# Performance work log

Hardware: AMD Instinct MI355X
Metric: run time of the kernel (lower is better)

The kernel has to match this reference:

```python
import jax, jax.numpy as jnp
import numpy as np

# Llama-2-7B-like GQA attention, prefill over packed equal-length sequences
H = 4096      # hidden_size
NH = 32       # num_attention_heads
NKV = 8       # num_key_value_heads
HD = H // NH  # head_dim = 128
B = 4         # number of packed sequences
S = 1024      # seq_len per sequence
T = B * S     # total packed tokens
BASE = 10000.0  # rope_theta


def setup_inputs() -> dict:
    key = jax.random.key(0)
    ks = jax.random.split(key, 5)
    x = jax.random.normal(ks[0], (T, H), jnp.float32)
    positions = jnp.tile(jnp.arange(S, dtype=jnp.int32), B)  # per-seq positions
    kv_cache = jnp.zeros((1,), jnp.float32)  # placeholder (prefill: kv from current tokens)
    init = 0.02
    wq = jax.random.normal(ks[1], (NH * HD, H), jnp.float32) * init
    wk = jax.random.normal(ks[2], (NKV * HD, H), jnp.float32) * init
    wv = jax.random.normal(ks[3], (NKV * HD, H), jnp.float32) * init
    wo = jax.random.normal(ks[4], (H, NH * HD), jnp.float32) * init
    return {"x": x, "positions": positions, "kv_cache": kv_cache,
            "wq": wq, "wk": wk, "wv": wv, "wo": wo, "seq_len": S}


def _rope(xh, cos_b, sin_b):
    # xh: [T, Hh, D]; cos_b/sin_b: [T, 1, D] (freqs repeat-interleaved by 2)
    half = xh.shape[-1] // 2
    x_rot = jnp.concatenate([-xh[..., half:], xh[..., :half]], axis=-1)
    return xh * cos_b + x_rot * sin_b


def reference(x, positions, kv_cache, wq, wk, wv, wo, seq_len):
    Tn = x.shape[0]
    q = (x @ wq.T).reshape(Tn, NH, HD)
    k = (x @ wk.T).reshape(Tn, NKV, HD)
    v = (x @ wv.T).reshape(Tn, NKV, HD)
    # GQA: repeat_interleave kv heads
    rep = NH // NKV
    k = jnp.repeat(k, rep, axis=1)
    v = jnp.repeat(v, rep, axis=1)
    # RoPE tables (faithful to _precompute_freqs/_rotary_embeddings)
    inv_freq = 1.0 / (BASE ** (jnp.arange(0, HD, 2, dtype=jnp.float32) / HD))
    t = jnp.arange(seq_len, dtype=jnp.float32)
    freqs = t[:, None] * inv_freq[None, :]            # [S, D/2]
    cos, sin = jnp.cos(freqs), jnp.sin(freqs)
    pos = jnp.clip(positions.astype(jnp.int32), 0, seq_len - 1)
    cos_b = jnp.repeat(cos[pos], 2, axis=-1)[:, None, :]  # [T,1,D]
    sin_b = jnp.repeat(sin[pos], 2, axis=-1)[:, None, :]
    q = _rope(q, cos_b, sin_b)
    k = _rope(k, cos_b, sin_b)
    # Paged attention (prefill): causal attention within each packed sequence
    Bn = Tn // seq_len
    qb = q.reshape(Bn, seq_len, NH, HD)
    kb = k.reshape(Bn, seq_len, NH, HD)
    vb = v.reshape(Bn, seq_len, NH, HD)
    scores = jnp.einsum('bqhd,bkhd->bhqk', qb, kb) * (HD ** -0.5)
    causal = jnp.tril(jnp.ones((seq_len, seq_len), bool))
    scores = jnp.where(causal[None, None], scores, -jnp.inf)
    probs = jax.nn.softmax(scores, axis=-1)
    out = jnp.einsum('bhqk,bkhd->bqhd', probs, vb).reshape(Tn, NH * HD)
    return out @ wo.T
```

## Files before the change

### kernel.cpp

```cpp
#include <hip/hip_runtime.h>
#include <hip/hip_bf16.h>
#include <math.h>

#define T_TOK 4096
#define HID   4096
#define NHQ   32
#define NKVH  8
#define HDIM  128
#define SEQ   1024
#define NBATCH 4

typedef __attribute__((ext_vector_type(8))) short bf16x8;
typedef __attribute__((ext_vector_type(4))) float f32x4;
typedef __attribute__((ext_vector_type(16))) float f32x16;

__device__ __forceinline__ unsigned short f2bf(float f) {
  union { float f; unsigned int u; } x; x.f = f;
  unsigned int r = x.u + 0x7FFFu + ((x.u >> 16) & 1u);
  return (unsigned short)(r >> 16);
}

#define GLOAD_LDS16(gp, lp)                                                        \
  __builtin_amdgcn_global_load_lds(                                                \
      (__attribute__((address_space(1))) void*)(unsigned long long)(const void*)(gp), \
      (__attribute__((address_space(3))) void*)(unsigned long long)(const void*)(lp), \
      16, 0, 0)

__global__ __launch_bounds__(256) void cast_all_k(const float* __restrict__ x,
                                                  const float* __restrict__ wq,
                                                  const float* __restrict__ wk,
                                                  const float* __restrict__ wv,
                                                  const float* __restrict__ wo,
                                                  unsigned short* __restrict__ xb,
                                                  unsigned short* __restrict__ wqkv,
                                                  unsigned short* __restrict__ wob) {
  int i = blockIdx.x * 256 + threadIdx.x;
  const float* src; unsigned short* dst; int off;
  if (i < 4194304)       { src = x;  dst = xb;   off = i; }
  else if (i < 8388608)  { src = wq; dst = wqkv; off = i - 4194304; }
  else if (i < 9437184)  { src = wk; dst = wqkv + 16777216; off = i - 8388608; }
  else if (i < 10485760) { src = wv; dst = wqkv + 20971520; off = i - 9437184; }
  else                   { src = wo; dst = wob;  off = i - 10485760; }
  float4 f = ((const float4*)src)[off];
  ushort4 o;
  o.x = f2bf(f.x); o.y = f2bf(f.y); o.z = f2bf(f.z); o.w = f2bf(f.w);
  ((ushort4*)dst)[off] = o;
}

template<bool FUSED>
__global__ __launch_bounds__(256) void gemm_core(const unsigned short* __restrict__ A,
                                                 const unsigned short* __restrict__ B,
                                                 float* __restrict__ C,
                                                 const int* __restrict__ pos,
                                                 unsigned short* __restrict__ qr,
                                                 unsigned short* __restrict__ kr,
                                                 unsigned short* __restrict__ vbuf,
                                                 int N, int K) {
  __shared__ unsigned short As[128][64];
  __shared__ unsigned short Bs[128][64];
  const int tid  = threadIdx.x;
  const int lane = tid & 63;
  const int wave = tid >> 6;
  const int half = lane >> 5;
  const int r31  = lane & 31;
  const int wm   = (wave >> 1) * 64;
  const int cb   = (wave & 1) * 32;
  const long rowBase = (long)blockIdx.y * 128;
  const long colBase = (long)blockIdx.x * 128;

  f32x16 acc[2][2] = {};

  for (int k0 = 0; k0 < K; k0 += 64) {
    __syncthreads();
#pragma unroll
    for (int it = 0; it < 4; ++it) {
      int c = it * 256 + tid;
      int row = c >> 3;
      int sg = (c & 7) ^ (row & 7);
      int ldsoff = (it * 256 + wave * 64) * 8;
      GLOAD_LDS16(A + (rowBase + row) * K + k0 + sg * 8, ((unsigned short*)As) + ldsoff);
      GLOAD_LDS16(B + (colBase + row) * K + k0 + sg * 8, ((unsigned short*)Bs) + ldsoff);
    }
    __syncthreads();
#pragma unroll
    for (int kk = 0; kk < 4; ++kk) {
      bf16x8 af[2], bfr[2];
#pragma unroll
      for (int i = 0; i < 2; ++i) {
        int row = wm + i * 32 + r31;
        af[i] = *(const bf16x8*)(&As[row][((kk * 2 + half) ^ (row & 7)) * 8]);
      }
#pragma unroll
      for (int j = 0; j < 2; ++j) {
        int row = cb + j * 64 + r31;
        bfr[j] = *(const bf16x8*)(&Bs[row][((kk * 2 + half) ^ (row & 7)) * 8]);
      }
#pragma unroll
      for (int i = 0; i < 2; ++i)
#pragma unroll
        for (int j = 0; j < 2; ++j)
          acc[i][j] = __builtin_amdgcn_mfma_f32_32x32x16_bf16(af[i], bfr[j], acc[i][j], 0, 0, 0);
    }
  }

  if (!FUSED) {
#pragma unroll
    for (int i = 0; i < 2; ++i)
#pragma unroll
      for (int j = 0; j < 2; ++j) {
        long c = colBase + cb + j * 64 + r31;
#pragma unroll
        for (int reg = 0; reg < 16; ++reg) {
          long row = rowBase + wm + i * 32 + 4 * half + (reg & 3) + 8 * (reg >> 2);
          C[row * N + c] = acc[i][j][reg];
        }
      }
    return;
  }

  const int n0 = (int)colBase;
  unsigned short* dst;
  int rstride, colofs;
  bool dorope;
  if (n0 < 4096)       { dst = qr;   rstride = NHQ * HDIM;  colofs = n0;        dorope = true; }
  else if (n0 < 5120)  { dst = kr;   rstride = NKVH * HDIM; colofs = n0 - 4096; dorope = true; }
  else                 { dst = vbuf; rstride = NKVH * HDIM; colofs = n0 - 5120; dorope = false; }
  const float c0 = -13.287712379549449f / 64.0f;
  const int d = cb + r31;
  const float f1 = exp2f(c0 * (float)(d >> 1));
  const float f2 = exp2f(c0 * (float)((d >> 1) + 32));
#pragma unroll
  for (int i = 0; i < 2; ++i) {
#pragma unroll
    for (int reg = 0; reg < 16; ++reg) {
      int grow = (int)rowBase + wm + i * 32 + 4 * half + (reg & 3) + 8 * (reg >> 2);
      unsigned short* drow = dst + (long)grow * rstride + colofs;
      float lo = acc[i][0][reg], hi = acc[i][1][reg];
      if (dorope) {
        int p = pos[grow];
        p = p < 0 ? 0 : (p > SEQ - 1 ? SEQ - 1 : p);
        float pf = (float)p;
        float s1, cc1, s2, cc2;
        __sincosf(pf * f1, &s1, &cc1);
        __sincosf(pf * f2, &s2, &cc2);
        drow[d]      = f2bf(lo * cc1 - hi * s1);
        drow[d + 64] = f2bf(hi * cc2 + lo * s2);
      } else {
        drow[d]      = f2bf(lo);
        drow[d + 64] = f2bf(hi);
      }
    }
  }
}

#define ATT_SCALE_L2 0.12754227022f
__global__ __launch_bounds__(256) void attn_k(const unsigned short* __restrict__ Qp,
                                              const unsigned short* __restrict__ Kp,
                                              const unsigned short* __restrict__ Vp,
                                              unsigned short* __restrict__ Op) {
  const int pr = blockIdx.x, h = blockIdx.y, b = blockIdx.z;
  const int kvh = h >> 2;
  const int tid = threadIdx.x, wave = tid >> 6, lane = tid & 63;
  const int m16 = lane & 15, quad = lane >> 4;

  __shared__ unsigned short Ks[64][128];
  __shared__ unsigned short Vt[128][64];
  __shared__ unsigned short Ps[4][32][64];

  for (int pass = 0; pass < 2; ++pass) {
    const int qt = pass ? pr : (7 - pr);
    const int qbase = qt * 128;
    const int wq_lo = qbase + wave * 32;

    bf16x8 qa[2][4];
#pragma unroll
    for (int i = 0; i < 2; ++i) {
      const unsigned short* qrow =
          Qp + (long)(b * SEQ + wq_lo + i * 16 + m16) * (NHQ * HDIM) + h * HDIM;
#pragma unroll
      for (int kk = 0; kk < 4; ++kk)
        qa[i][kk] = *(const bf16x8*)(qrow + kk * 32 + quad * 8);
    }

    f32x4 o[2][8] = {};
    float mrow[2][4], lrow[2][4];
#pragma unroll
    for (int i = 0; i < 2; ++i)
#pragma unroll
      for (int r = 0; r < 4; ++r) { mrow[i][r] = -1e30f; lrow[i][r] = 0.f; }

    const int nkt = qt * 2 + 2;
    for (int kt = 0; kt < nkt; ++kt) {
      __syncthreads();
      const unsigned short* Kbase =
          Kp + (long)(b * SEQ + kt * 64) * (NKVH * HDIM) + kvh * HDIM;
      const unsigned short* Vbase =
          Vp + (long)(b * SEQ + kt * 64) * (NKVH * HDIM) + kvh * HDIM;
#pragma unroll
      for (int it = 0; it < 4; ++it) {
        int c = it * 256 + tid;
        int row = c >> 4, psg = c & 15;
        int sg = (psg & 8) | ((psg & 7) ^ (row & 7));
        GLOAD_LDS16(Kbase + row * (NKVH * HDIM) + sg * 8,
                    ((unsigned short*)Ks) + (it * 256 + wave * 64) * 8);
      }
#pragma unroll
      for (int it = 0; it < 4; ++it) {
        int seg = it * 4 + wave;
        uint4 dv = *(const uint4*)(Vbase + lane * (NKVH * HDIM) + seg * 8);
        const unsigned short* pv = (const unsigned short*)&dv;
#pragma unroll
        for (int e = 0; e < 8; ++e) {
          int d = seg * 8 + e;
          Vt[d][((((lane >> 3) + d) & 7) * 8) + (lane & 7)] = pv[e];
        }
      }
      __syncthreads();

      const bool active = (kt * 64) <= (wq_lo + 31);
      if (active) {
        f32x4 s4[2][4] = {};
#pragma unroll
        for (int kk = 0; kk < 4; ++kk) {
          bf16x8 kbf[4];
#pragma unroll
          for (int j = 0; j < 4; ++j) {
            int row = j * 16 + m16;
            int cl = kk * 4 + quad;
            int ps = (cl & 8) | ((cl & 7) ^ (row & 7));
            kbf[j] = *(const bf16x8*)(&Ks[row][ps * 8]);
          }
#pragma unroll
          for (int i = 0; i < 2; ++i)
#pragma unroll
            for (int j = 0; j < 4; ++j)
              s4[i][j] = __builtin_amdgcn_mfma_f32_16x16x32_bf16(qa[i][kk], kbf[j], s4[i][j], 0, 0, 0);
        }
        const bool full = (kt * 64 + 63) <= wq_lo;
#pragma unroll
        for (int i = 0; i < 2; ++i) {
#pragma unroll
          for (int r = 0; r < 4; ++r) {
            const int qrow = i * 16 + quad * 4 + r;
            const int qi = qbase + wave * 32 + qrow;
            float v[4];
#pragma unroll
            for (int j = 0; j < 4; ++j) {
              v[j] = s4[i][j][r] * ATT_SCALE_L2;
              if (!full && (kt * 64 + j * 16 + m16 > qi)) v[j] = -1e30f;
            }
            float mx = fmaxf(fmaxf(v[0], v[1]), fmaxf(v[2], v[3]));
            mx = fmaxf(mx, __shfl_xor(mx, 1));
            mx = fmaxf(mx, __shfl_xor(mx, 2));
            mx = fmaxf(mx, __shfl_xor(mx, 4));
            mx = fmaxf(mx, __shfl_xor(mx, 8));
            float mold = mrow[i][r];
            float mnew = fmaxf(mold, mx);
            float alpha = exp2f(mold - mnew);
            float rs = 0.f;
#pragma unroll
            for (int j = 0; j < 4; ++j) {
              float pj = exp2f(v[j] - mnew);
              rs += pj;
              int col = j * 16 + m16;
              Ps[wave][qrow][((((col >> 3) + qrow) & 7) * 8) + (col & 7)] = f2bf(pj);
            }
            rs += __shfl_xor(rs, 1); rs += __shfl_xor(rs, 2);
            rs += __shfl_xor(rs, 4); rs += __shfl_xor(rs, 8);
            lrow[i][r] = lrow[i][r] * alpha + rs;
            mrow[i][r] = mnew;
#pragma unroll
            for (int n = 0; n < 8; ++n) o[i][n][r] *= alpha;
          }
        }
#pragma unroll
        for (int kk = 0; kk < 2; ++kk) {
          bf16x8 pa[2], vb[8];
#pragma unroll
          for (int i = 0; i < 2; ++i) {
            int row = i * 16 + m16;
            pa[i] = *(const bf16x8*)(&Ps[wave][row][(((kk * 4 + quad) + row) & 7) * 8]);
          }
#pragma unroll
          for (int n = 0; n < 8; ++n) {
            int row = n * 16 + m16;
            vb[n] = *(const bf16x8*)(&Vt[row][(((kk * 4 + quad) + row) & 7) * 8]);
          }
#pragma unroll
          for (int i = 0; i < 2; ++i)
#pragma unroll
            for (int n = 0; n < 8; ++n)
              o[i][n] = __builtin_amdgcn_mfma_f32_16x16x32_bf16(pa[i], vb[n], o[i][n], 0, 0, 0);
        }
      }
    }
#pragma unroll
    for (int i = 0; i < 2; ++i) {
#pragma unroll
      for (int r = 0; r < 4; ++r) {
        float inv = 1.0f / lrow[i][r];
        unsigned short* orow =
            Op + (long)(b * SEQ + wq_lo + i * 16 + quad * 4 + r) * (NHQ * HDIM) + h * HDIM;
#pragma unroll
        for (int n = 0; n < 8; ++n)
          orow[n * 16 + m16] = f2bf(o[i][n][r] * inv);
      }
    }
  }
}

extern "C" void kernel_launch(void* const* d_in, const int* in_sizes, int n_in,
                              void* d_out, int out_size, void* d_ws, size_t ws_size,
                              hipStream_t stream) {
  (void)in_sizes; (void)n_in; (void)out_size; (void)ws_size;
  const float* x  = (const float*)d_in[0];
  const int* pos  = (const int*)d_in[1];
  const float* wq = (const float*)d_in[3];
  const float* wk = (const float*)d_in[4];
  const float* wv = (const float*)d_in[5];
  const float* wo = (const float*)d_in[6];
  float* out = (float*)d_out;

  char* ws = (char*)d_ws;
  unsigned short* xb    = (unsigned short*)(ws);
  unsigned short* wqkv  = (unsigned short*)(ws + (32ll << 20));
  unsigned short* wob   = (unsigned short*)(ws + (80ll << 20));
  unsigned short* qr    = (unsigned short*)(ws + (112ll << 20));
  unsigned short* kr    = (unsigned short*)(ws + (144ll << 20));
  unsigned short* vb_   = (unsigned short*)(ws + (152ll << 20));
  unsigned short* ao    = (unsigned short*)(ws + (160ll << 20));

  cast_all_k<<<57344, 256, 0, stream>>>(x, wq, wk, wv, wo, xb, wqkv, wob);
  gemm_core<true><<<dim3(48, 32), 256, 0, stream>>>(xb, wqkv, nullptr, pos, qr, kr, vb_, 6144, 4096);
  attn_k<<<dim3(4, 32, 4), 256, 0, stream>>>(qr, kr, vb_, ao);
  gemm_core<false><<<dim3(32, 32), 256, 0, stream>>>(ao, wob, out, nullptr, nullptr, nullptr, nullptr, 4096, 4096);
}
```

Before: 808.6 us.

## Rewrite GEMMs as 256x256 tiles with triple-buffered async LDS pipeline

Replaces the 128x128 single-buffered GEMM with a 512-thread, 256x256-tile kernel that uses a 3-stage LDS ring with K-step 32. Global-to-LDS loads are issued two stages ahead and split across the two MFMA halves. It also adds an XCD-aware workgroup swizzle and s_setprio around the MFMA bursts. The aim is to hide global load latency behind compute and to raise arithmetic intensity per tile. The cost is higher register and LDS pressure, and fewer workgroups (384 and 256), which may underfill the 256 CUs.

```diff
diff --git a/kernel.cpp b/kernel.cpp
--- a/kernel.cpp
+++ b/kernel.cpp
@@ -48,77 +48,140 @@
 }
 
 template<bool FUSED>
-__global__ __launch_bounds__(256) void gemm_core(const unsigned short* __restrict__ A,
-                                                 const unsigned short* __restrict__ B,
-                                                 float* __restrict__ C,
-                                                 const int* __restrict__ pos,
-                                                 unsigned short* __restrict__ qr,
-                                                 unsigned short* __restrict__ kr,
-                                                 unsigned short* __restrict__ vbuf,
-                                                 int N, int K) {
-  __shared__ unsigned short As[128][64];
-  __shared__ unsigned short Bs[128][64];
+__global__ __launch_bounds__(512, 2) void gemm8(const unsigned short* __restrict__ A,
+                                                const unsigned short* __restrict__ B,
+                                                float* __restrict__ C,
+                                                const int* __restrict__ pos,
+                                                unsigned short* __restrict__ qr,
+                                                unsigned short* __restrict__ kr,
+                                                unsigned short* __restrict__ vbuf,
+                                                int N, int K) {
+  __shared__ unsigned short As3[3][8192];
+  __shared__ unsigned short Bs3[3][8192];
   const int tid  = threadIdx.x;
   const int lane = tid & 63;
   const int wave = tid >> 6;
   const int half = lane >> 5;
   const int r31  = lane & 31;
-  const int wm   = (wave >> 1) * 64;
-  const int cb   = (wave & 1) * 32;
-  const long rowBase = (long)blockIdx.y * 128;
-  const long colBase = (long)blockIdx.x * 128;
-
-  f32x16 acc[2][2] = {};
-
-  for (int k0 = 0; k0 < K; k0 += 64) {
-    __syncthreads();
-#pragma unroll
-    for (int it = 0; it < 4; ++it) {
-      int c = it * 256 + tid;
-      int row = c >> 3;
-      int sg = (c & 7) ^ (row & 7);
-      int ldsoff = (it * 256 + wave * 64) * 8;
-      GLOAD_LDS16(A + (rowBase + row) * K + k0 + sg * 8, ((unsigned short*)As) + ldsoff);
-      GLOAD_LDS16(B + (colBase + row) * K + k0 + sg * 8, ((unsigned short*)Bs) + ldsoff);
-    }
-    __syncthreads();
-#pragma unroll
-    for (int kk = 0; kk < 4; ++kk) {
-      bf16x8 af[2], bfr[2];
-#pragma unroll
-      for (int i = 0; i < 2; ++i) {
-        int row = wm + i * 32 + r31;
-        af[i] = *(const bf16x8*)(&As[row][((kk * 2 + half) ^ (row & 7)) * 8]);
-      }
+  const int wml  = (wave >> 2) * 128;
+  const int wn   = wave & 3;
+  const int cbl  = (wn & 1) * 32 + (wn >> 1) * 128;
+
+  const int gx = gridDim.x;
+  const int nwg = gx * gridDim.y;
+  const int orig = blockIdx.y * gx + blockIdx.x;
+  const int swz = (orig & 7) * (nwg >> 3) + (orig >> 3);
+  const long rowBase = (long)(swz / gx) * 256;
+  const long colBase = (long)(swz % gx) * 256;
+
+  const int sr64 = tid >> 3;
+  const int sj   = tid & 7;
+  const int scg  = ((sj & 3) ^ (sr64 & 3)) * 8;
+  const long srow = (long)(sr64 * 2 + (sj >> 2));
+  const unsigned short* srcA0 = A + (rowBase + srow) * (long)K + scg;
+  const unsigned short* srcA1 = srcA0 + 128 * (long)K;
+  const unsigned short* srcB0 = B + (colBase + srow) * (long)K + scg;
+  const unsigned short* srcB1 = srcB0 + 128 * (long)K;
+  const int dH0 = (wave * 8) * 64;
+  const int dH1 = (64 + wave * 8) * 64;
+
+  f32x16 acc[4][2] = {};
+  const int nt = K >> 5;
+
+  GLOAD_LDS16(srcA0,      &As3[0][dH0]);
+  GLOAD_LDS16(srcA1,      &As3[0][dH1]);
+  GLOAD_LDS16(srcB0,      &Bs3[0][dH0]);
+  GLOAD_LDS16(srcB1,      &Bs3[0][dH1]);
+  GLOAD_LDS16(srcA0 + 32, &As3[1][dH0]);
+  GLOAD_LDS16(srcA1 + 32, &As3[1][dH1]);
+  GLOAD_LDS16(srcB0 + 32, &Bs3[1][dH0]);
+  GLOAD_LDS16(srcB1 + 32, &Bs3[1][dH1]);
+  asm volatile("s_waitcnt vmcnt(4)" ::: "memory");
+  __builtin_amdgcn_s_barrier();
+
+  int q = 0, qs = 2;
+  for (int t = 0; t < nt; ++t) {
+    if (t) {
+      if (t + 1 < nt) asm volatile("s_waitcnt vmcnt(4)" ::: "memory");
+      else            asm volatile("s_waitcnt vmcnt(0)" ::: "memory");
+      __builtin_amdgcn_s_barrier();
+    }
+    const unsigned short* Aq = &As3[q][0];
+    const unsigned short* Bq = &Bs3[q][0];
+    const bool doStage = (t + 2) < nt;
+    const int koff = (t + 2) * 32;
+
+    bf16x8 af[4], bfr[2];
+#pragma unroll
+    for (int i = 0; i < 4; ++i) {
+      int r = wml + i * 32 + r31;
+      int r64 = r >> 1;
+      af[i] = *(const bf16x8*)(Aq + r64 * 64 + (r & 1) * 32 + ((half ^ (r64 & 3)) * 8));
+    }
+#pragma unroll
+    for (int j = 0; j < 2; ++j) {
+      int r = cbl + j * 64 + r31;
+      int r64 = r >> 1;
+      bfr[j] = *(const bf16x8*)(Bq + r64 * 64 + (r & 1) * 32 + ((half ^ (r64 & 3)) * 8));
+    }
+    if (doStage) {
+      GLOAD_LDS16(srcA0 + koff, &As3[qs][dH0]);
+      GLOAD_LDS16(srcA1 + koff, &As3[qs][dH1]);
+    }
+    __builtin_amdgcn_s_barrier();
+    __builtin_amdgcn_s_setprio(1);
+#pragma unroll
+    for (int i = 0; i < 4; ++i)
+#pragma unroll
+      for (int j = 0; j < 2; ++j)
+        acc[i][j] = __builtin_amdgcn_mfma_f32_32x32x16_bf16(af[i], bfr[j], acc[i][j], 0, 0, 0);
+    __builtin_amdgcn_s_setprio(0);
+
+#pragma unroll
+    for (int i = 0; i < 4; ++i) {
+      int r = wml + i * 32 + r31;
+      int r64 = r >> 1;
+      af[i] = *(const bf16x8*)(Aq + r64 * 64 + (r & 1) * 32 + (((2 + half) ^ (r64 & 3)) * 8));
+    }
+#pragma unroll
+    for (int j = 0; j < 2; ++j) {
+      int r = cbl + j * 64 + r31;
+      int r64 = r >> 1;
+      bfr[j] = *(const bf16x8*)(Bq + r64 * 64 + (r & 1) * 32 + (((2 + half) ^ (r64 & 3)) * 8));
+    }
+    if (doStage) {
+      GLOAD_LDS16(srcB0 + koff, &Bs3[qs][dH0]);
+      GLOAD_LDS16(srcB1 + koff, &Bs3[qs][dH1]);
+    }
+    __builtin_amdgcn_s_barrier();
+    __builtin_amdgcn_s_setprio(1);
+#pragma unroll
+    for (int i = 0; i < 4; ++i)
+#pragma unroll
+      for (int j = 0; j < 2; ++j)
+        acc[i][j] = __builtin_amdgcn_mfma_f32_32x32x16_bf16(af[i], bfr[j], acc[i][j], 0, 0, 0);
+    __builtin_amdgcn_s_setprio(0);
+
+    q  = (q  == 2) ? 0 : q + 1;
+    qs = (qs == 2) ? 0 : qs + 1;
+  }
+
+  if (!FUSED) {
+#pragma unroll
+    for (int i = 0; i < 4; ++i)
 #pragma unroll
       for (int j = 0; j < 2; ++j) {
-        int row = cb + j * 64 + r31;
-        bfr[j] = *(const bf16x8*)(&Bs[row][((kk * 2 + half) ^ (row & 7)) * 8]);
-      }
-#pragma unroll
-      for (int i = 0; i < 2; ++i)
-#pragma unroll
-        for (int j = 0; j < 2; ++j)
-          acc[i][j] = __builtin_amdgcn_mfma_f32_32x32x16_bf16(af[i], bfr[j], acc[i][j], 0, 0, 0);
-    }
-  }
-
-  if (!FUSED) {
-#pragma unroll
-    for (int i = 0; i < 2; ++i)
-#pragma unroll
-      for (int j = 0; j < 2; ++j) {
-        long c = colBase + cb + j * 64 + r31;
+        long c = colBase + cbl + j * 64 + r31;
 #pragma unroll
         for (int reg = 0; reg < 16; ++reg) {
-          long row = rowBase + wm + i * 32 + 4 * half + (reg & 3) + 8 * (reg >> 2);
+          long row = rowBase + wml + i * 32 + 4 * half + (reg & 3) + 8 * (reg >> 2);
           C[row * N + c] = acc[i][j][reg];
         }
       }
     return;
   }
 
-  const int n0 = (int)colBase;
+  const int n0 = (int)colBase + (cbl & 128);
   unsigned short* dst;
   int rstride, colofs;
   bool dorope;
@@ -126,14 +189,14 @@
   else if (n0 < 5120)  { dst = kr;   rstride = NKVH * HDIM; colofs = n0 - 4096; dorope = true; }
   else                 { dst = vbuf; rstride = NKVH * HDIM; colofs = n0 - 5120; dorope = false; }
   const float c0 = -13.287712379549449f / 64.0f;
-  const int d = cb + r31;
+  const int d = (cbl & 127) + r31;
   const float f1 = exp2f(c0 * (float)(d >> 1));
   const float f2 = exp2f(c0 * (float)((d >> 1) + 32));
 #pragma unroll
-  for (int i = 0; i < 2; ++i) {
+  for (int i = 0; i < 4; ++i) {
 #pragma unroll
     for (int reg = 0; reg < 16; ++reg) {
-      int grow = (int)rowBase + wm + i * 32 + 4 * half + (reg & 3) + 8 * (reg >> 2);
+      int grow = (int)rowBase + wml + i * 32 + 4 * half + (reg & 3) + 8 * (reg >> 2);
       unsigned short* drow = dst + (long)grow * rstride + colofs;
       float lo = acc[i][0][reg], hi = acc[i][1][reg];
       if (dorope) {
@@ -331,7 +394,7 @@
   unsigned short* ao    = (unsigned short*)(ws + (160ll << 20));
 
   cast_all_k<<<57344, 256, 0, stream>>>(x, wq, wk, wv, wo, xb, wqkv, wob);
-  gemm_core<true><<<dim3(48, 32), 256, 0, stream>>>(xb, wqkv, nullptr, pos, qr, kr, vb_, 6144, 4096);
+  gemm8<true><<<dim3(24, 16), 512, 0, stream>>>(xb, wqkv, nullptr, pos, qr, kr, vb_, 6144, 4096);
   attn_k<<<dim3(4, 32, 4), 256, 0, stream>>>(qr, kr, vb_, ao);
-  gemm_core<false><<<dim3(32, 32), 256, 0, stream>>>(ao, wob, out, nullptr, nullptr, nullptr, nullptr, 4096, 4096);
+  gemm8<false><<<dim3(16, 16), 512, 0, stream>>>(ao, wob, out, nullptr, nullptr, nullptr, nullptr, 4096, 4096);
 }
```

Result: no change. 812.3 us (+0.5%).

## Rewrite GEMM as 8-wave 256x128 tile with triple-buffered LDS pipeline

Applied to the files above, without the earlier changes.

Replaces the 128x128 single-buffered GEMM with a 512-thread, 256x128-tile kernel. It uses a three-slot LDS ring, prefetches two k-steps ahead with split global-to-LDS stages, and relies on explicit waitcnt and barriers plus setprio around the MFMA blocks. It switches to 16x16x32 MFMAs and swizzles the workgroup order for L2 locality. The RoPE and plain-store epilogues are remapped to the new accumulator layout. The aim is to hide load latency and raise MFMA utilization in both projection GEMMs, at the cost of more LDS per block and fragile hand-counted wait values.

```diff
diff --git a/kernel.cpp b/kernel.cpp
--- a/kernel.cpp
+++ b/kernel.cpp
@@ -12,7 +12,6 @@
 
 typedef __attribute__((ext_vector_type(8))) short bf16x8;
 typedef __attribute__((ext_vector_type(4))) float f32x4;
-typedef __attribute__((ext_vector_type(16))) float f32x16;
 
 __device__ __forceinline__ unsigned short f2bf(float f) {
   union { float f; unsigned int u; } x; x.f = f;
@@ -48,71 +47,122 @@
 }
 
 template<bool FUSED>
-__global__ __launch_bounds__(256) void gemm_core(const unsigned short* __restrict__ A,
-                                                 const unsigned short* __restrict__ B,
-                                                 float* __restrict__ C,
-                                                 const int* __restrict__ pos,
-                                                 unsigned short* __restrict__ qr,
-                                                 unsigned short* __restrict__ kr,
-                                                 unsigned short* __restrict__ vbuf,
-                                                 int N, int K) {
-  __shared__ unsigned short As[128][64];
-  __shared__ unsigned short Bs[128][64];
+__global__ __launch_bounds__(512, 2) void gemm8(const unsigned short* __restrict__ A,
+                                                const unsigned short* __restrict__ B,
+                                                float* __restrict__ C,
+                                                const int* __restrict__ pos,
+                                                unsigned short* __restrict__ qr,
+                                                unsigned short* __restrict__ kr,
+                                                unsigned short* __restrict__ vbuf,
+                                                int N, int K) {
+  __shared__ unsigned short As[3][16384];
+  __shared__ unsigned short Bs[3][8192];
   const int tid  = threadIdx.x;
   const int lane = tid & 63;
   const int wave = tid >> 6;
-  const int half = lane >> 5;
-  const int r31  = lane & 31;
-  const int wm   = (wave >> 1) * 64;
-  const int cb   = (wave & 1) * 32;
-  const long rowBase = (long)blockIdx.y * 128;
-  const long colBase = (long)blockIdx.x * 128;
-
-  f32x16 acc[2][2] = {};
-
-  for (int k0 = 0; k0 < K; k0 += 64) {
-    __syncthreads();
-#pragma unroll
-    for (int it = 0; it < 4; ++it) {
-      int c = it * 256 + tid;
-      int row = c >> 3;
-      int sg = (c & 7) ^ (row & 7);
-      int ldsoff = (it * 256 + wave * 64) * 8;
-      GLOAD_LDS16(A + (rowBase + row) * K + k0 + sg * 8, ((unsigned short*)As) + ldsoff);
-      GLOAD_LDS16(B + (colBase + row) * K + k0 + sg * 8, ((unsigned short*)Bs) + ldsoff);
-    }
-    __syncthreads();
-#pragma unroll
-    for (int kk = 0; kk < 4; ++kk) {
-      bf16x8 af[2], bfr[2];
-#pragma unroll
-      for (int i = 0; i < 2; ++i) {
-        int row = wm + i * 32 + r31;
-        af[i] = *(const bf16x8*)(&As[row][((kk * 2 + half) ^ (row & 7)) * 8]);
-      }
-#pragma unroll
-      for (int j = 0; j < 2; ++j) {
-        int row = cb + j * 64 + r31;
-        bfr[j] = *(const bf16x8*)(&Bs[row][((kk * 2 + half) ^ (row & 7)) * 8]);
-      }
-#pragma unroll
-      for (int i = 0; i < 2; ++i)
-#pragma unroll
-        for (int j = 0; j < 2; ++j)
-          acc[i][j] = __builtin_amdgcn_mfma_f32_32x32x16_bf16(af[i], bfr[j], acc[i][j], 0, 0, 0);
-    }
+  const int m16  = lane & 15;
+  const int quad = lane >> 4;
+  const int wm   = wave >> 1;
+  const int wn   = wave & 1;
+
+  const int gx = gridDim.x;
+  const int nwg = gx * gridDim.y;
+  const int orig = blockIdx.y * gx + blockIdx.x;
+  const int swz = (orig & 7) * (nwg >> 3) + (orig >> 3);
+  const long rowBase = (long)(swz / gx) * 256;
+  const long colBase = (long)(swz % gx) * 128;
+
+  const long Kl = K;
+  const int sck = ((tid & 7) ^ (((tid >> 5) & 1) << 1)) * 8;
+  const unsigned short* sA = A + (rowBase + (tid >> 3)) * Kl + sck;
+  const unsigned short* sB = B + (colBase + (tid >> 3)) * Kl + sck;
+  const int dofs = wave * 512;
+
+#define STG_A01(sl_, ko_) { GLOAD_LDS16(sA + (ko_),           &As[sl_][dofs]);          \
+                            GLOAD_LDS16(sA + (ko_) + 64*Kl,   &As[sl_][4096 + dofs]); }
+#define STG_A23(sl_, ko_) { GLOAD_LDS16(sA + (ko_) + 128*Kl,  &As[sl_][8192 + dofs]);   \
+                            GLOAD_LDS16(sA + (ko_) + 192*Kl,  &As[sl_][12288 + dofs]); }
+#define STG_B01(sl_, ko_) { GLOAD_LDS16(sB + (ko_),           &Bs[sl_][dofs]);          \
+                            GLOAD_LDS16(sB + (ko_) + 64*Kl,   &Bs[sl_][4096 + dofs]); }
+
+#define RDA(dv_, mfr_, ks_) {                                                     \
+    int row_ = wm * 64 + (mfr_) * 16 + m16;                                       \
+    dv_ = *(const bf16x8*)(Aq + row_ * 64 + ((((ks_)*4 + quad)*8) ^ ((row_ & 4) << 2))); }
+#define RDB(dv_, nf_, ks_) {                                                      \
+    int row_ = wn * 32 + ((nf_) & 1) * 16 + ((nf_) >> 1) * 64 + m16;              \
+    dv_ = *(const bf16x8*)(Bq + row_ * 64 + ((((ks_)*4 + quad)*8) ^ ((row_ & 4) << 2))); }
+
+  f32x4 acc[4][4] = {};
+  const int nt = K >> 6;
+
+  STG_A01(0, 0); STG_A23(0, 0); STG_B01(0, 0);
+  STG_A01(1, 64); STG_A23(1, 64); STG_B01(1, 64);
+  asm volatile("s_waitcnt vmcnt(6)" ::: "memory");
+  __builtin_amdgcn_s_barrier();
+
+  int sl = 0;
+  for (int t = 0; t < nt; ++t) {
+    const unsigned short* Aq = &As[sl][0];
+    const unsigned short* Bq = &Bs[sl][0];
+    const int s2 = sl >= 1 ? sl - 1 : 2;
+    const bool doStage = (t + 2) < nt;
+    const long ko = (long)(t + 2) * 64;
+
+    bf16x8 af[2][2], bf[4][2];
+#pragma unroll
+    for (int mf = 0; mf < 2; ++mf)
+#pragma unroll
+      for (int ks = 0; ks < 2; ++ks) RDA(af[mf][ks], mf, ks);
+#pragma unroll
+    for (int nf = 0; nf < 4; ++nf)
+#pragma unroll
+      for (int ks = 0; ks < 2; ++ks) RDB(bf[nf][ks], nf, ks);
+    if (doStage) STG_A01(s2, ko);
+    asm volatile("s_waitcnt lgkmcnt(8)" ::: "memory");
+    __builtin_amdgcn_s_barrier();
+    __builtin_amdgcn_s_setprio(1);
+#pragma unroll
+    for (int mf = 0; mf < 2; ++mf)
+#pragma unroll
+      for (int nf = 0; nf < 4; ++nf)
+#pragma unroll
+        for (int ks = 0; ks < 2; ++ks)
+          acc[mf][nf] = __builtin_amdgcn_mfma_f32_16x16x32_bf16(af[mf][ks], bf[nf][ks], acc[mf][nf], 0, 0, 0);
+    __builtin_amdgcn_s_setprio(0);
+    __builtin_amdgcn_s_barrier();
+
+#pragma unroll
+    for (int mf = 0; mf < 2; ++mf)
+#pragma unroll
+      for (int ks = 0; ks < 2; ++ks) RDA(af[mf][ks], 2 + mf, ks);
+    if (doStage) { STG_A23(s2, ko); STG_B01(s2, ko); }
+    if (doStage)         asm volatile("s_waitcnt vmcnt(6)" ::: "memory");
+    else if (t + 1 < nt) asm volatile("s_waitcnt vmcnt(0)" ::: "memory");
+    __builtin_amdgcn_s_barrier();
+    __builtin_amdgcn_s_setprio(1);
+#pragma unroll
+    for (int mf = 0; mf < 2; ++mf)
+#pragma unroll
+      for (int nf = 0; nf < 4; ++nf)
+#pragma unroll
+        for (int ks = 0; ks < 2; ++ks)
+          acc[2 + mf][nf] = __builtin_amdgcn_mfma_f32_16x16x32_bf16(af[mf][ks], bf[nf][ks], acc[2 + mf][nf], 0, 0, 0);
+    __builtin_amdgcn_s_setprio(0);
+    __builtin_amdgcn_s_barrier();
+
+    sl = sl == 2 ? 0 : sl + 1;
   }
 
   if (!FUSED) {
 #pragma unroll
-    for (int i = 0; i < 2; ++i)
-#pragma unroll
-      for (int j = 0; j < 2; ++j) {
-        long c = colBase + cb + j * 64 + r31;
-#pragma unroll
-        for (int reg = 0; reg < 16; ++reg) {
-          long row = rowBase + wm + i * 32 + 4 * half + (reg & 3) + 8 * (reg >> 2);
-          C[row * N + c] = acc[i][j][reg];
+    for (int mf = 0; mf < 4; ++mf)
+#pragma unroll
+      for (int nf = 0; nf < 4; ++nf) {
+        long c = colBase + wn * 32 + (nf & 1) * 16 + (nf >> 1) * 64 + m16;
+#pragma unroll
+        for (int reg = 0; reg < 4; ++reg) {
+          long row = rowBase + wm * 64 + mf * 16 + quad * 4 + reg;
+          C[row * N + c] = acc[mf][nf][reg];
         }
       }
     return;
@@ -126,28 +176,40 @@
   else if (n0 < 5120)  { dst = kr;   rstride = NKVH * HDIM; colofs = n0 - 4096; dorope = true; }
   else                 { dst = vbuf; rstride = NKVH * HDIM; colofs = n0 - 5120; dorope = false; }
   const float c0 = -13.287712379549449f / 64.0f;
-  const int d = cb + r31;
-  const float f1 = exp2f(c0 * (float)(d >> 1));
-  const float f2 = exp2f(c0 * (float)((d >> 1) + 32));
-#pragma unroll
-  for (int i = 0; i < 2; ++i) {
-#pragma unroll
-    for (int reg = 0; reg < 16; ++reg) {
-      int grow = (int)rowBase + wm + i * 32 + 4 * half + (reg & 3) + 8 * (reg >> 2);
+  float fA[2], fB[2];
+#pragma unroll
+  for (int e = 0; e < 2; ++e) {
+    int d = wn * 32 + e * 16 + m16;
+    fA[e] = exp2f(c0 * (float)(d >> 1));
+    fB[e] = exp2f(c0 * (float)((d >> 1) + 32));
+  }
+#pragma unroll
+  for (int mf = 0; mf < 4; ++mf) {
+#pragma unroll
+    for (int reg = 0; reg < 4; ++reg) {
+      int grow = (int)rowBase + wm * 64 + mf * 16 + quad * 4 + reg;
       unsigned short* drow = dst + (long)grow * rstride + colofs;
-      float lo = acc[i][0][reg], hi = acc[i][1][reg];
       if (dorope) {
         int p = pos[grow];
         p = p < 0 ? 0 : (p > SEQ - 1 ? SEQ - 1 : p);
         float pf = (float)p;
-        float s1, cc1, s2, cc2;
-        __sincosf(pf * f1, &s1, &cc1);
-        __sincosf(pf * f2, &s2, &cc2);
-        drow[d]      = f2bf(lo * cc1 - hi * s1);
-        drow[d + 64] = f2bf(hi * cc2 + lo * s2);
+#pragma unroll
+        for (int e = 0; e < 2; ++e) {
+          int d = wn * 32 + e * 16 + m16;
+          float lo = acc[mf][e][reg], hi = acc[mf][e + 2][reg];
+          float s1, cc1, s2, cc2;
+          __sincosf(pf * fA[e], &s1, &cc1);
+          __sincosf(pf * fB[e], &s2, &cc2);
+          drow[d]      = f2bf(lo * cc1 - hi * s1);
+          drow[d + 64] = f2bf(hi * cc2 + lo * s2);
+        }
       } else {
-        drow[d]      = f2bf(lo);
-        drow[d + 64] = f2bf(hi);
+#pragma unroll
+        for (int e = 0; e < 2; ++e) {
+          int d = wn * 32 + e * 16 + m16;
+          drow[d]      = f2bf(acc[mf][e][reg]);
+          drow[d + 64] = f2bf(acc[mf][e + 2][reg]);
+        }
       }
     }
   }
@@ -331,7 +393,7 @@
   unsigned short* ao    = (unsigned short*)(ws + (160ll << 20));
 
   cast_all_k<<<57344, 256, 0, stream>>>(x, wq, wk, wv, wo, xb, wqkv, wob);
-  gemm_core<true><<<dim3(48, 32), 256, 0, stream>>>(xb, wqkv, nullptr, pos, qr, kr, vb_, 6144, 4096);
+  gemm8<true><<<dim3(48, 16), 512, 0, stream>>>(xb, wqkv, nullptr, pos, qr, kr, vb_, 6144, 4096);
   attn_k<<<dim3(4, 32, 4), 256, 0, stream>>>(qr, kr, vb_, ao);
-  gemm_core<false><<<dim3(32, 32), 256, 0, stream>>>(ao, wob, out, nullptr, nullptr, nullptr, nullptr, 4096, 4096);
-}
+  gemm8<false><<<dim3(32, 16), 512, 0, stream>>>(ao, wob, out, nullptr, nullptr, nullptr, nullptr, 4096, 4096);
+}
```

After: 810.7 us. Within noise of the previous version (+0.3%).
